# Optimization experiments

Measured on AMD Instinct MI355X. Metric: run time of the kernel, lower is better.

The kernel has to match this reference:

```python
import jax, jax.numpy as jnp
import numpy as np

NB_USERS = 100000
NB_MOVIES = 20000
K = 64
N = 2000000
MAX_RATING = 5.0


def setup_inputs() -> dict:
    key = jax.random.key(0)
    ks = jax.random.split(key, 8)
    return {
        "x_users": jnp.arange(NB_USERS, dtype=jnp.int32),  # every user queried once -> original's user filter is identity
        "x_movies": jax.random.randint(ks[0], (NB_USERS,), 0, NB_MOVIES),
        "data_users": jax.random.randint(ks[1], (N,), 0, NB_USERS),
        "data_movies": jax.random.randint(ks[2], (N,), 0, NB_MOVIES),
        "data_ratings": jax.random.uniform(ks[3], (N,), dtype=jnp.float32) * MAX_RATING,
        "movies_features": jax.random.normal(ks[4], (NB_MOVIES, K), dtype=jnp.float32),
        "W_r": jax.random.normal(ks[5], (K, 1), dtype=jnp.float32) * 0.1,
        "b_r": jnp.zeros((K,), dtype=jnp.float32),
        "W_c": jax.random.normal(ks[6], (K, K), dtype=jnp.float32) * 0.1,
        "b_c": jnp.zeros((K,), dtype=jnp.float32),
        "w_out": jax.random.normal(ks[7], (1, 1), dtype=jnp.float32),
        "b_out": jnp.zeros((1,), dtype=jnp.float32),
    }


def reference(x_users, x_movies, data_users, data_movies, data_ratings,
              movies_features, W_r, b_r, W_c, b_c, w_out, b_out):
    # movies_ratings_func: Linear(1,k) + sigmoid on normalized ratings
    ratings = jax.nn.sigmoid((data_ratings[:, None] / MAX_RATING) @ W_r.T + b_r)  # [N,k]
    # combined_func: Linear(k,k) + sigmoid on (gathered movie feats * rating emb)
    rbm = jax.nn.sigmoid((movies_features[data_movies] * ratings) @ W_c.T + b_c)  # [N,k]
    # scatter-add aggregate per user
    rating_by_user = jax.ops.segment_sum(rbm, data_users, num_segments=NB_USERS)  # [U,k]
    nb_ratings = jax.ops.segment_sum(jnp.ones((N,), dtype=rbm.dtype), data_users,
                                     num_segments=NB_USERS)  # [U]
    # ignore_if_seen=True path (faithful, including rbm indexed by movie id as in original)
    rating_by_user = rating_by_user.at[x_users].add(-rbm[x_movies])
    nb_ratings = nb_ratings.at[x_users].set(jnp.maximum(jnp.float32(1.0), nb_ratings[x_users] - 1.0))
    user_features = rating_by_user[x_users] / nb_ratings[x_users][:, None]  # [B,k]
    movie_features = movies_features[x_movies]  # [B,k]
    r = (movie_features * user_features).mean(-1, keepdims=True)  # [B,1]
    r = (r @ w_out.T + b_out) * MAX_RATING  # result_func then *max_rating
    return r.reshape(-1)
```

## Files before the change

### kernel.cpp

```cpp
#include <hip/hip_runtime.h>

#define NB_USERS 100000
#define NB_MOVIES 20000
#define KDIM 64
#define NPTS 2000000
#define NTILES (NPTS / 64)
#define RQ_LEVELS 8192
#define UPB 128
#define NBUCK 782
#define CHUNK 8192
#define NCHUNK ((NPTS + CHUNK - 1) / CHUNK)
#define BCAP 3584
#define LOG2E 1.44269504088896f

#define MF_N (NB_MOVIES * KDIM)
#define RT_N ((RQ_LEVELS + 1) * KDIM)

typedef _Float16 f16x8 __attribute__((ext_vector_type(8)));
typedef float    f32x4 __attribute__((ext_vector_type(4)));

__device__ __forceinline__ float sigmoidf(float z) {
    return 1.0f / (1.0f + __expf(-z));
}
__device__ __forceinline__ float sigmoid_w(float w) {
    return __builtin_amdgcn_rcpf(1.0f + __builtin_amdgcn_exp2f(w));
}

__global__ __launch_bounds__(256) void prep_kernel(
    const float* __restrict__ mf, const float* __restrict__ W_r,
    const float* __restrict__ b_r, const float* __restrict__ W_c,
    _Float16* __restrict__ mf16, _Float16* __restrict__ rtab16,
    _Float16* __restrict__ wcfrag)
{
    const int idx = blockIdx.x * 256 + threadIdx.x;
    if (idx < MF_N) {
        mf16[idx] = (_Float16)mf[idx];
    } else if (idx < MF_N + RT_N) {
        const int i = idx - MF_N;
        const int q = i >> 6, k = i & 63;
        rtab16[i] = (_Float16)sigmoidf(fmaf((float)q * (1.0f / RQ_LEVELS), W_r[k], b_r[k]));
    } else if (idx < MF_N + RT_N + 512) {
        const int i = idx - MF_N - RT_N;
        const int ntkt = i >> 6;
        const int nt = ntkt >> 1, kt = ntkt & 1;
        const int lane = i & 63;
        const float* src = &W_c[(nt * 16 + (lane & 15)) * KDIM + kt * 32 + (lane >> 4) * 8];
        _Float16* dst = wcfrag + (size_t)ntkt * 512 + lane * 8;
        #pragma unroll
        for (int e = 0; e < 8; ++e) dst[e] = (_Float16)(src[e] * -LOG2E);
    }
}

__global__ __launch_bounds__(1024) void bucket_hist_kernel(
    const int* __restrict__ du, int* __restrict__ bhist)
{
    __shared__ int h[NBUCK];
    for (int b = threadIdx.x; b < NBUCK; b += 1024) h[b] = 0;
    __syncthreads();
    int i = blockIdx.x * 1024 + threadIdx.x;
    const int stride = gridDim.x * 1024;
    for (; i < NPTS; i += stride) atomicAdd(&h[du[i] >> 7], 1);
    __syncthreads();
    for (int b = threadIdx.x; b < NBUCK; b += 1024)
        if (h[b]) atomicAdd(&bhist[b], h[b]);
}

__global__ __launch_bounds__(256) void bscan_kernel(
    const int* __restrict__ bhist, int* __restrict__ bstart, int* __restrict__ bcursor)
{
    __shared__ int scn[256];
    const int t = threadIdx.x;
    int c[4];
    int s = 0;
    #pragma unroll
    for (int j = 0; j < 4; ++j) {
        const int idx = t * 4 + j;
        c[j] = (idx < NBUCK) ? bhist[idx] : 0;
        s += c[j];
    }
    scn[t] = s;
    __syncthreads();
    for (int d = 1; d < 256; d <<= 1) {
        const int a = (t >= d) ? scn[t - d] : 0;
        __syncthreads();
        scn[t] += a;
        __syncthreads();
    }
    int run = scn[t] - s;
    #pragma unroll
    for (int j = 0; j < 4; ++j) {
        const int idx = t * 4 + j;
        if (idx < NBUCK) { bstart[idx] = run; bcursor[idx] = run; }
        run += c[j];
    }
}

__global__ __launch_bounds__(1024, 2) void binA_kernel(
    const int* __restrict__ du, const int* __restrict__ dm,
    const float* __restrict__ dr,
    int* __restrict__ bcursor, uint2* __restrict__ binned)
{
    __shared__ uint2 buf[CHUNK];
    __shared__ int cnt[NBUCK];
    __shared__ int scn[1024];
    __shared__ int sbase[NBUCK];
    __shared__ int cur[NBUCK];
    __shared__ int gbase[NBUCK];

    const int t  = threadIdx.x;
    const int c0 = blockIdx.x * CHUNK;
    const int n  = min(CHUNK, NPTS - c0);

    for (int b = t; b < NBUCK; b += 1024) cnt[b] = 0;
    __syncthreads();

    for (int i = t; i < n; i += 1024)
        atomicAdd(&cnt[(unsigned)du[c0 + i] >> 7], 1);
    __syncthreads();

    const int cv = (t < NBUCK) ? cnt[t] : 0;
    scn[t] = cv;
    __syncthreads();
    for (int d = 1; d < 1024; d <<= 1) {
        const int a = (t >= d) ? scn[t - d] : 0;
        __syncthreads();
        scn[t] += a;
        __syncthreads();
    }
    if (t < NBUCK) {
        const int e = scn[t] - cv;
        sbase[t] = e;
        cur[t]   = e;
        if (cv > 0) gbase[t] = atomicAdd(&bcursor[t], cv);
    }
    __syncthreads();

    for (int i = t; i < n; i += 1024) {
        const unsigned u  = (unsigned)du[c0 + i];
        const unsigned m  = (unsigned)dm[c0 + i];
        const unsigned rq = (unsigned)(int)fmaf(dr[c0 + i], (float)RQ_LEVELS / 5.0f, 0.5f);
        const int pos = atomicAdd(&cur[u >> 7], 1);
        buf[pos] = make_uint2((u << 15) | m, rq);
    }
    __syncthreads();

    for (int i = t; i < n; i += 1024) {
        const uint2 q = buf[i];
        const int b = q.x >> 22;
        binned[gbase[b] + (i - sbase[b])] = q;
    }
}

__global__ __launch_bounds__(256) void binB_kernel(
    const uint2* __restrict__ binned,
    const int* __restrict__ bhist, const int* __restrict__ bstart,
    uint2* __restrict__ sorted, float* __restrict__ nbrf)
{
    __shared__ uint2 buf[BCAP];
    __shared__ int cnt[UPB];
    __shared__ int cur[UPB];

    const int t  = threadIdx.x;
    const int b  = blockIdx.x;
    const int n  = bhist[b];
    const int s0 = bstart[b];

    if (t < UPB) cnt[t] = 0;
    __syncthreads();

    for (int i = t; i < n; i += 256)
        atomicAdd(&cnt[(binned[s0 + i].x >> 15) & (UPB - 1)], 1);
    __syncthreads();

    const int uid = b * UPB + t;
    if (t < UPB && uid < NB_USERS) nbrf[uid] = (float)cnt[t];

    const int inc = (t < UPB) ? cnt[t] : 0;
    if (t < UPB) cur[t] = inc;
    __syncthreads();
    for (int d = 1; d < UPB; d <<= 1) {
        const int a = (t < UPB && t >= d) ? cur[t - d] : 0;
        __syncthreads();
        if (t < UPB) cur[t] += a;
        __syncthreads();
    }
    if (t < UPB) cur[t] -= inc;
    __syncthreads();

    for (int i = t; i < n; i += 256) {
        const uint2 q  = binned[s0 + i];
        const int  lu  = (q.x >> 15) & (UPB - 1);
        const int  pos = atomicAdd(&cur[lu], 1);
        buf[pos] = q;
    }
    __syncthreads();

    for (int i = t; i < n; i += 256)
        sorted[s0 + i] = buf[i];
}

__global__ __launch_bounds__(256) void rbm_saved_kernel(
    const int* __restrict__ dm, const float* __restrict__ dr,
    const _Float16* __restrict__ mf16, const _Float16* __restrict__ rtab16,
    const _Float16* __restrict__ wcfrag, const float* __restrict__ b_c,
    float* __restrict__ rbm_saved)
{
    __shared__ _Float16 bsh[8 * 512];
    for (int i = threadIdx.x; i < 512; i += 256)
        ((f16x8*)bsh)[i] = ((const f16x8*)wcfrag)[i];
    __syncthreads();

    const int lane = threadIdx.x & 63;
    const int wave = blockIdx.x * (blockDim.x >> 6) + (threadIdx.x >> 6);
    const int NT = (NB_MOVIES + 63) / 64;
    if (wave >= NT) return;

    float wbcv[4];
    #pragma unroll
    for (int nt = 0; nt < 4; ++nt) wbcv[nt] = -LOG2E * b_c[nt * 16 + (lane & 15)];

    const int base = wave * 64;
    const int koff = (lane >> 4) * 8;

    #pragma unroll 1
    for (int mt = 0; mt < 4; ++mt) {
        const int pg = base + mt * 16 + (lane & 15);
        int   m = 0;
        float r = 0.f;
        if (pg < NB_MOVIES) { m = dm[pg]; r = dr[pg]; }
        const int rq = (int)fmaf(r, (float)RQ_LEVELS / 5.0f, 0.5f);

        const f16x8 ma = *(const f16x8*)(mf16   + (size_t)m  * KDIM + koff);
        const f16x8 mb = *(const f16x8*)(mf16   + (size_t)m  * KDIM + 32 + koff);
        const f16x8 ta = *(const f16x8*)(rtab16 + (size_t)rq * KDIM + koff);
        const f16x8 tb = *(const f16x8*)(rtab16 + (size_t)rq * KDIM + 32 + koff);
        const f16x8 a0 = ma * ta;
        const f16x8 a1 = mb * tb;

        f32x4 acc[4];
        #pragma unroll
        for (int nt = 0; nt < 4; ++nt) {
            const f16x8 b0 = *(const f16x8*)(bsh + (nt * 2 + 0) * 512 + lane * 8);
            const f16x8 b1 = *(const f16x8*)(bsh + (nt * 2 + 1) * 512 + lane * 8);
            acc[nt] = (f32x4){0.f, 0.f, 0.f, 0.f};
            acc[nt] = __builtin_amdgcn_mfma_f32_16x16x32_f16(a0, b0, acc[nt], 0, 0, 0);
            acc[nt] = __builtin_amdgcn_mfma_f32_16x16x32_f16(a1, b1, acc[nt], 0, 0, 0);
        }

        #pragma unroll
        for (int reg = 0; reg < 4; ++reg) {
            const int prow_g = base + mt * 16 + (lane >> 4) * 4 + reg;
            if (prow_g < NB_MOVIES) {
                #pragma unroll
                for (int nt = 0; nt < 4; ++nt) {
                    const float rbm = sigmoid_w(acc[nt][reg] + wbcv[nt]);
                    rbm_saved[(size_t)prow_g * KDIM + nt * 16 + (lane & 15)] = rbm;
                }
            }
        }
    }
}

__global__ __launch_bounds__(256, 4) void phase1_sorted_kernel(
    const uint2* __restrict__ sorted_ur,
    const _Float16* __restrict__ mf16,
    const _Float16* __restrict__ rtab16,
    const _Float16* __restrict__ wcfrag,
    const float* __restrict__ b_c,
    float* __restrict__ rbu)
{
    __shared__ _Float16 bsh[8 * 512];
    for (int i = threadIdx.x; i < 512; i += 256)
        ((f16x8*)bsh)[i] = ((const f16x8*)wcfrag)[i];
    __syncthreads();

    const int lane = threadIdx.x & 63;
    const int wave = blockIdx.x * (blockDim.x >> 6) + (threadIdx.x >> 6);
    const int nwav = gridDim.x * (blockDim.x >> 6);

    float wbcv[4];
    #pragma unroll
    for (int nt = 0; nt < 4; ++nt) wbcv[nt] = -LOG2E * b_c[nt * 16 + (lane & 15)];

    const int koff = (lane >> 4) * 8;
    const int g    = lane >> 4;

    for (int it = wave; it < NTILES; it += nwav) {
        const int base = it * 64;

        #pragma unroll 1
        for (int mt = 0; mt < 4; ++mt) {
            const uint2 ur = sorted_ur[base + mt * 16 + (lane & 15)];
            const unsigned u_at = ur.x >> 15;
            const int      m    = (int)(ur.x & 0x7fffu);
            const int      rq   = (int)ur.y;

            const f16x8 ma = *(const f16x8*)(mf16   + (size_t)m  * KDIM + koff);
            const f16x8 mb = *(const f16x8*)(mf16   + (size_t)m  * KDIM + 32 + koff);
            const f16x8 ta = *(const f16x8*)(rtab16 + (size_t)rq * KDIM + koff);
            const f16x8 tb = *(const f16x8*)(rtab16 + (size_t)rq * KDIM + 32 + koff);
            const f16x8 a0 = ma * ta;
            const f16x8 a1 = mb * tb;

            f32x4 acc[4];
            #pragma unroll
            for (int nt = 0; nt < 4; ++nt) {
                const f16x8 b0 = *(const f16x8*)(bsh + (nt * 2 + 0) * 512 + lane * 8);
                const f16x8 b1 = *(const f16x8*)(bsh + (nt * 2 + 1) * 512 + lane * 8);
                acc[nt] = (f32x4){0.f, 0.f, 0.f, 0.f};
                acc[nt] = __builtin_amdgcn_mfma_f32_16x16x32_f16(a0, b0, acc[nt], 0, 0, 0);
                acc[nt] = __builtin_amdgcn_mfma_f32_16x16x32_f16(a1, b1, acc[nt], 0, 0, 0);
            }

            #pragma unroll
            for (int nt = 0; nt < 4; ++nt)
                #pragma unroll
                for (int reg = 0; reg < 4; ++reg)
                    acc[nt][reg] = sigmoid_w(acc[nt][reg] + wbcv[nt]);

            const unsigned u_prev =
                (unsigned)__shfl((int)u_at, lane - 1, 64);
            const bool boundary = ((lane & 15) == 0) || (u_at != u_prev);
            unsigned long long bm = __ballot(boundary) & 0xFFFFull;

            while (bm) {
                const int s = __builtin_ctzll(bm);
                bm &= bm - 1;
                const int e = bm ? __builtin_ctzll(bm) : 16;
                const unsigned useg =
                    (unsigned)__builtin_amdgcn_readlane((int)u_at, s);

                const int lo = s - g * 4;
                const int hi = e - g * 4;
                float p0 = 0.f, p1 = 0.f, p2 = 0.f, p3 = 0.f;
                #pragma unroll
                for (int reg = 0; reg < 4; ++reg) {
                    const bool in = (reg >= lo) && (reg < hi);
                    p0 += in ? acc[0][reg] : 0.f;
                    p1 += in ? acc[1][reg] : 0.f;
                    p2 += in ? acc[2][reg] : 0.f;
                    p3 += in ? acc[3][reg] : 0.f;
                }
                p0 += __shfl_xor(p0, 16, 64); p0 += __shfl_xor(p0, 32, 64);
                p1 += __shfl_xor(p1, 16, 64); p1 += __shfl_xor(p1, 32, 64);
                p2 += __shfl_xor(p2, 16, 64); p2 += __shfl_xor(p2, 32, 64);
                p3 += __shfl_xor(p3, 16, 64); p3 += __shfl_xor(p3, 32, 64);

                const float v01 = (g & 1) ? p1 : p0;
                const float v23 = (g & 1) ? p3 : p2;
                const float val = (g & 2) ? v23 : v01;
                atomicAdd(&rbu[(size_t)useg * KDIM + lane], val);
            }
        }
    }
}

__global__ __launch_bounds__(256) void phase2_kernel(
    const int* __restrict__ x_users,
    const int* __restrict__ x_movies,
    const float* __restrict__ mf,
    const float* __restrict__ rbu,
    const float* __restrict__ nbrf,
    const float* __restrict__ rbm_saved,
    const float* __restrict__ w_out,
    const float* __restrict__ b_out,
    float* __restrict__ out)
{
    const int lane = threadIdx.x & 63;
    const int wave = blockIdx.x * (blockDim.x >> 6) + (threadIdx.x >> 6);
    if (wave >= NB_USERS) return;

    const int u  = x_users[wave];
    const int xm = x_movies[wave];

    const float nb = fmaxf(1.0f, nbrf[u] - 1.0f);
    const float uf = (rbu[(size_t)u * KDIM + lane] -
                      rbm_saved[(size_t)xm * KDIM + lane]) / nb;
    float p = mf[(size_t)xm * KDIM + lane] * uf;

    #pragma unroll
    for (int off = 32; off > 0; off >>= 1)
        p += __shfl_xor(p, off, 64);

    if (lane == 0)
        out[wave] = (p * (1.0f / 64.0f) * w_out[0] + b_out[0]) * 5.0f;
}

extern "C" void kernel_launch(void* const* d_in, const int* in_sizes, int n_in,
                              void* d_out, int out_size, void* d_ws, size_t ws_size,
                              hipStream_t stream) {
    const int*   x_users      = (const int*)  d_in[0];
    const int*   x_movies     = (const int*)  d_in[1];
    const int*   data_users   = (const int*)  d_in[2];
    const int*   data_movies  = (const int*)  d_in[3];
    const float* data_ratings = (const float*)d_in[4];
    const float* mf           = (const float*)d_in[5];
    const float* W_r          = (const float*)d_in[6];
    const float* b_r          = (const float*)d_in[7];
    const float* W_c          = (const float*)d_in[8];
    const float* b_c          = (const float*)d_in[9];
    const float* w_out        = (const float*)d_in[10];
    const float* b_out        = (const float*)d_in[11];
    float* out = (float*)d_out;

    float*     rbu       = (float*)d_ws;
    uint2*     binned    = (uint2*)d_ws;
    float*     nbrf      = rbu + (size_t)NB_USERS * KDIM;
    float*     rbm_saved = nbrf + NB_USERS;
    uint2*     sorted_ur = (uint2*)(rbm_saved + (size_t)NB_MOVIES * KDIM);
    _Float16*  mf16      = (_Float16*)(sorted_ur + NPTS);
    _Float16*  rtab16    = mf16 + (size_t)MF_N;
    _Float16*  wcfrag    = rtab16 + (size_t)RT_N;
    int*       bhist     = (int*)(wcfrag + 8 * 512);
    int*       bstart    = bhist + NBUCK;
    int*       bcursor   = bstart + NBUCK;

    hipMemsetAsync(bhist, 0, NBUCK * sizeof(int), stream);

    prep_kernel<<<(MF_N + RT_N + 512 + 255) / 256, 256, 0, stream>>>(
        mf, W_r, b_r, W_c, mf16, rtab16, wcfrag);

    bucket_hist_kernel<<<512, 1024, 0, stream>>>(data_users, bhist);
    bscan_kernel<<<1, 256, 0, stream>>>(bhist, bstart, bcursor);

    binA_kernel<<<NCHUNK, 1024, 0, stream>>>(
        data_users, data_movies, data_ratings, bcursor, binned);

    rbm_saved_kernel<<<79, 256, 0, stream>>>(
        data_movies, data_ratings, mf16, rtab16, wcfrag, b_c, rbm_saved);

    binB_kernel<<<NBUCK, 256, 0, stream>>>(binned, bhist, bstart, sorted_ur, nbrf);

    hipMemsetAsync(rbu, 0, (size_t)NB_USERS * KDIM * sizeof(float), stream);

    phase1_sorted_kernel<<<2048, 256, 0, stream>>>(
        sorted_ur, mf16, rtab16, wcfrag, b_c, rbu);

    phase2_kernel<<<(NB_USERS * 64 + 255) / 256, 256, 0, stream>>>(
        x_users, x_movies, mf, rbu, nbrf, rbm_saved, w_out, b_out, out);
}
```

Baseline: 169.9 us.

## Fuse prep and bucket histogram kernels, widen binB blocks, fold bias into MFMA init

```diff
diff --git a/kernel.cpp b/kernel.cpp
--- a/kernel.cpp
+++ b/kernel.cpp
@@ -15,6 +15,8 @@
 
 #define MF_N (NB_MOVIES * KDIM)
 #define RT_N ((RQ_LEVELS + 1) * KDIM)
+#define PREP_BLOCKS ((MF_N + RT_N + 512 + 255) / 256)
+#define HIST_BLOCKS 2048
 
 typedef _Float16 f16x8 __attribute__((ext_vector_type(8)));
 typedef float    f32x4 __attribute__((ext_vector_type(4)));
@@ -26,43 +28,43 @@
     return __builtin_amdgcn_rcpf(1.0f + __builtin_amdgcn_exp2f(w));
 }
 
-__global__ __launch_bounds__(256) void prep_kernel(
+__global__ __launch_bounds__(256) void prep_hist_kernel(
     const float* __restrict__ mf, const float* __restrict__ W_r,
     const float* __restrict__ b_r, const float* __restrict__ W_c,
+    const int* __restrict__ du,
     _Float16* __restrict__ mf16, _Float16* __restrict__ rtab16,
-    _Float16* __restrict__ wcfrag)
-{
-    const int idx = blockIdx.x * 256 + threadIdx.x;
-    if (idx < MF_N) {
-        mf16[idx] = (_Float16)mf[idx];
-    } else if (idx < MF_N + RT_N) {
-        const int i = idx - MF_N;
-        const int q = i >> 6, k = i & 63;
-        rtab16[i] = (_Float16)sigmoidf(fmaf((float)q * (1.0f / RQ_LEVELS), W_r[k], b_r[k]));
-    } else if (idx < MF_N + RT_N + 512) {
-        const int i = idx - MF_N - RT_N;
-        const int ntkt = i >> 6;
-        const int nt = ntkt >> 1, kt = ntkt & 1;
-        const int lane = i & 63;
-        const float* src = &W_c[(nt * 16 + (lane & 15)) * KDIM + kt * 32 + (lane >> 4) * 8];
-        _Float16* dst = wcfrag + (size_t)ntkt * 512 + lane * 8;
-        #pragma unroll
-        for (int e = 0; e < 8; ++e) dst[e] = (_Float16)(src[e] * -LOG2E);
-    }
-}
-
-__global__ __launch_bounds__(1024) void bucket_hist_kernel(
-    const int* __restrict__ du, int* __restrict__ bhist)
-{
-    __shared__ int h[NBUCK];
-    for (int b = threadIdx.x; b < NBUCK; b += 1024) h[b] = 0;
-    __syncthreads();
-    int i = blockIdx.x * 1024 + threadIdx.x;
-    const int stride = gridDim.x * 1024;
-    for (; i < NPTS; i += stride) atomicAdd(&h[du[i] >> 7], 1);
-    __syncthreads();
-    for (int b = threadIdx.x; b < NBUCK; b += 1024)
-        if (h[b]) atomicAdd(&bhist[b], h[b]);
+    _Float16* __restrict__ wcfrag, int* __restrict__ bhist)
+{
+    if (blockIdx.x < PREP_BLOCKS) {
+        const int idx = blockIdx.x * 256 + threadIdx.x;
+        if (idx < MF_N) {
+            mf16[idx] = (_Float16)mf[idx];
+        } else if (idx < MF_N + RT_N) {
+            const int i = idx - MF_N;
+            const int q = i >> 6, k = i & 63;
+            rtab16[i] = (_Float16)sigmoidf(fmaf((float)q * (1.0f / RQ_LEVELS), W_r[k], b_r[k]));
+        } else if (idx < MF_N + RT_N + 512) {
+            const int i = idx - MF_N - RT_N;
+            const int ntkt = i >> 6;
+            const int nt = ntkt >> 1, kt = ntkt & 1;
+            const int lane = i & 63;
+            const float* src = &W_c[(nt * 16 + (lane & 15)) * KDIM + kt * 32 + (lane >> 4) * 8];
+            _Float16* dst = wcfrag + (size_t)ntkt * 512 + lane * 8;
+            #pragma unroll
+            for (int e = 0; e < 8; ++e) dst[e] = (_Float16)(src[e] * -LOG2E);
+        }
+    } else {
+        __shared__ int h[NBUCK];
+        for (int b = threadIdx.x; b < NBUCK; b += 256) h[b] = 0;
+        __syncthreads();
+        const int hb = blockIdx.x - PREP_BLOCKS;
+        int i = hb * 256 + threadIdx.x;
+        const int stride = HIST_BLOCKS * 256;
+        for (; i < NPTS; i += stride) atomicAdd(&h[du[i] >> 7], 1);
+        __syncthreads();
+        for (int b = threadIdx.x; b < NBUCK; b += 256)
+            if (h[b]) atomicAdd(&bhist[b], h[b]);
+    }
 }
 
 __global__ __launch_bounds__(256) void bscan_kernel(
@@ -151,7 +153,7 @@
     }
 }
 
-__global__ __launch_bounds__(256) void binB_kernel(
+__global__ __launch_bounds__(512) void binB_kernel(
     const uint2* __restrict__ binned,
     const int* __restrict__ bhist, const int* __restrict__ bstart,
     uint2* __restrict__ sorted, float* __restrict__ nbrf)
@@ -168,7 +170,7 @@
     if (t < UPB) cnt[t] = 0;
     __syncthreads();
 
-    for (int i = t; i < n; i += 256)
+    for (int i = t; i < n; i += 512)
         atomicAdd(&cnt[(binned[s0 + i].x >> 15) & (UPB - 1)], 1);
     __syncthreads();
 
@@ -187,7 +189,7 @@
     if (t < UPB) cur[t] -= inc;
     __syncthreads();
 
-    for (int i = t; i < n; i += 256) {
+    for (int i = t; i < n; i += 512) {
         const uint2 q  = binned[s0 + i];
         const int  lu  = (q.x >> 15) & (UPB - 1);
         const int  pos = atomicAdd(&cur[lu], 1);
@@ -195,7 +197,7 @@
     }
     __syncthreads();
 
-    for (int i = t; i < n; i += 256)
+    for (int i = t; i < n; i += 512)
         sorted[s0 + i] = buf[i];
 }
 
@@ -242,7 +244,7 @@
         for (int nt = 0; nt < 4; ++nt) {
             const f16x8 b0 = *(const f16x8*)(bsh + (nt * 2 + 0) * 512 + lane * 8);
             const f16x8 b1 = *(const f16x8*)(bsh + (nt * 2 + 1) * 512 + lane * 8);
-            acc[nt] = (f32x4){0.f, 0.f, 0.f, 0.f};
+            acc[nt] = (f32x4){wbcv[nt], wbcv[nt], wbcv[nt], wbcv[nt]};
             acc[nt] = __builtin_amdgcn_mfma_f32_16x16x32_f16(a0, b0, acc[nt], 0, 0, 0);
             acc[nt] = __builtin_amdgcn_mfma_f32_16x16x32_f16(a1, b1, acc[nt], 0, 0, 0);
         }
@@ -253,7 +255,7 @@
             if (prow_g < NB_MOVIES) {
                 #pragma unroll
                 for (int nt = 0; nt < 4; ++nt) {
-                    const float rbm = sigmoid_w(acc[nt][reg] + wbcv[nt]);
+                    const float rbm = sigmoid_w(acc[nt][reg]);
                     rbm_saved[(size_t)prow_g * KDIM + nt * 16 + (lane & 15)] = rbm;
                 }
             }
@@ -307,7 +309,7 @@
             for (int nt = 0; nt < 4; ++nt) {
                 const f16x8 b0 = *(const f16x8*)(bsh + (nt * 2 + 0) * 512 + lane * 8);
                 const f16x8 b1 = *(const f16x8*)(bsh + (nt * 2 + 1) * 512 + lane * 8);
-                acc[nt] = (f32x4){0.f, 0.f, 0.f, 0.f};
+                acc[nt] = (f32x4){wbcv[nt], wbcv[nt], wbcv[nt], wbcv[nt]};
                 acc[nt] = __builtin_amdgcn_mfma_f32_16x16x32_f16(a0, b0, acc[nt], 0, 0, 0);
                 acc[nt] = __builtin_amdgcn_mfma_f32_16x16x32_f16(a1, b1, acc[nt], 0, 0, 0);
             }
@@ -316,7 +318,7 @@
             for (int nt = 0; nt < 4; ++nt)
                 #pragma unroll
                 for (int reg = 0; reg < 4; ++reg)
-                    acc[nt][reg] = sigmoid_w(acc[nt][reg] + wbcv[nt]);
+                    acc[nt][reg] = sigmoid_w(acc[nt][reg]);
 
             const unsigned u_prev =
                 (unsigned)__shfl((int)u_at, lane - 1, 64);
@@ -417,10 +419,9 @@
 
     hipMemsetAsync(bhist, 0, NBUCK * sizeof(int), stream);
 
-    prep_kernel<<<(MF_N + RT_N + 512 + 255) / 256, 256, 0, stream>>>(
-        mf, W_r, b_r, W_c, mf16, rtab16, wcfrag);
-
-    bucket_hist_kernel<<<512, 1024, 0, stream>>>(data_users, bhist);
+    prep_hist_kernel<<<PREP_BLOCKS + HIST_BLOCKS, 256, 0, stream>>>(
+        mf, W_r, b_r, W_c, data_users, mf16, rtab16, wcfrag, bhist);
+
     bscan_kernel<<<1, 256, 0, stream>>>(bhist, bstart, bcursor);
 
     binA_kernel<<<NCHUNK, 1024, 0, stream>>>(
@@ -429,7 +430,7 @@
     rbm_saved_kernel<<<79, 256, 0, stream>>>(
         data_movies, data_ratings, mf16, rtab16, wcfrag, b_c, rbm_saved);
 
-    binB_kernel<<<NBUCK, 256, 0, stream>>>(binned, bhist, bstart, sorted_ur, nbrf);
+    binB_kernel<<<NBUCK, 512, 0, stream>>>(binned, bhist, bstart, sorted_ur, nbrf);
 
     hipMemsetAsync(rbu, 0, (size_t)NB_USERS * KDIM * sizeof(float), stream);
 
```

Result: slower. 202.5 us (+19.2%).
